# Kernel tuning notes

Hardware: AMD Instinct MI355X
Metric: run time of the kernel (lower is better)

Reference implementation:

```python
import jax, jax.numpy as jnp
import numpy as np
from jax import lax

B, L, D, H = 2, 4096, 1024, 16
K = 4            # short conv kernel size
HD = D // H      # head dim = 64
EPS = 1e-5


def causal_dw_conv(x, w):
    # depthwise causal conv: x [B,L,D], w [D,K]
    xp = jnp.pad(x, ((0, 0), (K - 1, 0), (0, 0)))
    out = xp[:, 0:L, :] * w[:, 0]
    for j in range(1, K):
        out = out + xp[:, j:j + L, :] * w[:, j]
    return out


def setup_inputs() -> dict:
    key = jax.random.key(0)
    ks = jax.random.split(key, 10)
    s = 0.02
    return {
        "hidden_states": jax.random.normal(ks[0], (B, L, D), jnp.float32),
        "Wq": jax.random.normal(ks[1], (D, D), jnp.float32) * s,
        "Wk": jax.random.normal(ks[2], (D, D), jnp.float32) * s,
        "Wv": jax.random.normal(ks[3], (D, D), jnp.float32) * s,
        "Wb": jax.random.normal(ks[4], (D, H), jnp.float32) * s,
        "conv_q": jax.random.normal(ks[5], (D, K), jnp.float32) * s,
        "conv_k": jax.random.normal(ks[6], (D, K), jnp.float32) * s,
        "conv_v": jax.random.normal(ks[7], (D, K), jnp.float32) * s,
        "o_norm_w": jnp.ones((HD,), jnp.float32),
        "Wo": jax.random.normal(ks[8], (D, D), jnp.float32) * s,
    }


def reference(hidden_states, Wq, Wk, Wv, Wb, conv_q, conv_k, conv_v, o_norm_w, Wo):
    x = hidden_states
    # projections + short causal conv with SiLU (qk_activation == 'silu')
    q = jax.nn.silu(causal_dw_conv(x @ Wq, conv_q))
    k = jax.nn.silu(causal_dw_conv(x @ Wk, conv_k))
    v = jax.nn.silu(causal_dw_conv(x @ Wv, conv_v))

    # [B,L,D] -> [L,B,H,hd] for the time scan
    def to_heads(t):
        return t.reshape(B, L, H, HD).transpose(1, 0, 2, 3)

    q, k, v = to_heads(q), to_heads(k), to_heads(v)

    # l2 qk-norm
    q = q / jnp.linalg.norm(q, axis=-1, keepdims=True)
    k = k / jnp.linalg.norm(k, axis=-1, keepdims=True)

    # beta gate [L,B,H]
    beta = jax.nn.sigmoid(x @ Wb).transpose(1, 0, 2)

    def step(S, inp):
        qt, kt, vt, bt = inp  # [B,H,hd] x3, [B,H]
        v_old = jnp.einsum('bhk,bhkv->bhv', kt, S)
        delta = (vt - v_old) * bt[..., None]
        S = S + jnp.einsum('bhk,bhv->bhkv', kt, delta)
        ot = jnp.einsum('bhk,bhkv->bhv', qt, S)
        return S, ot

    S0 = jnp.zeros((B, H, HD, HD), x.dtype)
    _, o = lax.scan(step, S0, (q, k, v, beta))  # o: [L,B,H,hd]
    o = o.transpose(1, 0, 2, 3)  # [B,L,H,hd]

    # per-head RMSNorm
    rms = jax.lax.rsqrt(jnp.mean(o * o, axis=-1, keepdims=True) + EPS)
    o = o * rms * o_norm_w

    return o.reshape(B, L, D) @ Wo
```

## Files before the change

### kernel.cpp

```cpp
#include <hip/hip_runtime.h>
#include <hip/hip_bf16.h>
#include <math.h>

#define BB 2
#define LL 4096
#define DD 1024
#define HH 16
#define HDIM 64
#define CC 64
#define NC 64
#define BH 32
#define GG 8
#define GS 8

typedef __attribute__((ext_vector_type(8))) short short8;
typedef __attribute__((ext_vector_type(4))) float f32x4;
typedef unsigned short u16;
typedef unsigned int u32;

__device__ __forceinline__ u16 f2bf(float f) {
    unsigned int u = __float_as_uint(f);
    unsigned int r = (u + 0x7fffu + ((u >> 16) & 1u)) >> 16;
    return (u16)r;
}
__device__ __forceinline__ float bf2f(u16 h) {
    return __uint_as_float((unsigned)h << 16);
}
__device__ __forceinline__ void split2(float x, u16& h, u16& l) {
    h = f2bf(x);
    l = f2bf(x - bf2f(h));
}
__device__ __forceinline__ u32 packhl(float x) {
    u16 h, l; split2(x, h, l);
    return (u32)h | ((u32)l << 16);
}
__device__ __forceinline__ float unpackhl(u32 v) {
    return bf2f((u16)v) + bf2f((u16)(v >> 16));
}
__device__ __forceinline__ float4 ld_bf4(const u16* p) {
    uint2 v = *(const uint2*)p;
    return make_float4(bf2f((u16)v.x), bf2f((u16)(v.x >> 16)),
                       bf2f((u16)v.y), bf2f((u16)(v.y >> 16)));
}

__device__ __forceinline__ void gld_lds16(const void* g, void* l) {
    __builtin_amdgcn_global_load_lds(
        (const __attribute__((address_space(1))) void*)g,
        (__attribute__((address_space(3))) void*)l, 16, 0, 0);
}

__device__ __forceinline__ int swz(int r, int c) {
    return (r << 6) + ((((c >> 2) ^ (r >> 2)) & 15) << 2) + (c & 3);
}
__device__ __forceinline__ int swze(int r, int c) {
    return (r << 6) + (c ^ (((r ^ (r >> 3)) & 7) << 3));
}

__device__ __forceinline__ void mm64(const u16* __restrict__ Ah, const u16* __restrict__ Al,
                                     const u16* __restrict__ Bh, const u16* __restrict__ Bl,
                                     f32x4* acc, int w, int lane) {
    const int ln = lane & 15, kg = (lane >> 4) * 8;
#pragma unroll
    for (int kb = 0; kb < 2; ++kb) {
        const int k0 = kb * 32 + kg;
        short8 ah = *(const short8*)&Ah[swze(w * 16 + ln, k0)];
        short8 al = *(const short8*)&Al[swze(w * 16 + ln, k0)];
#pragma unroll
        for (int j = 0; j < 4; ++j) {
            short8 bh = *(const short8*)&Bh[swze(j * 16 + ln, k0)];
            short8 bl = *(const short8*)&Bl[swze(j * 16 + ln, k0)];
            acc[j] = __builtin_amdgcn_mfma_f32_16x16x32_bf16(ah, bh, acc[j], 0, 0, 0);
            acc[j] = __builtin_amdgcn_mfma_f32_16x16x32_bf16(ah, bl, acc[j], 0, 0, 0);
            acc[j] = __builtin_amdgcn_mfma_f32_16x16x32_bf16(al, bh, acc[j], 0, 0, 0);
        }
    }
}
__device__ __forceinline__ void mm64_bb(const u16* __restrict__ Ah,
                                        const u16* __restrict__ Bh,
                                        f32x4* acc, int w, int lane) {
    const int ln = lane & 15, kg = (lane >> 4) * 8;
#pragma unroll
    for (int kb = 0; kb < 2; ++kb) {
        const int k0 = kb * 32 + kg;
        short8 ah = *(const short8*)&Ah[swze(w * 16 + ln, k0)];
#pragma unroll
        for (int j = 0; j < 4; ++j) {
            short8 bh = *(const short8*)&Bh[swze(j * 16 + ln, k0)];
            acc[j] = __builtin_amdgcn_mfma_f32_16x16x32_bf16(ah, bh, acc[j], 0, 0, 0);
        }
    }
}
__device__ __forceinline__ void mm64_ab(const u16* __restrict__ Ah,
                                        const u16* __restrict__ Bh, const u16* __restrict__ Bl,
                                        f32x4* acc, int w, int lane) {
    const int ln = lane & 15, kg = (lane >> 4) * 8;
#pragma unroll
    for (int kb = 0; kb < 2; ++kb) {
        const int k0 = kb * 32 + kg;
        short8 ah = *(const short8*)&Ah[swze(w * 16 + ln, k0)];
#pragma unroll
        for (int j = 0; j < 4; ++j) {
            short8 bh = *(const short8*)&Bh[swze(j * 16 + ln, k0)];
            short8 bl = *(const short8*)&Bl[swze(j * 16 + ln, k0)];
            acc[j] = __builtin_amdgcn_mfma_f32_16x16x32_bf16(ah, bh, acc[j], 0, 0, 0);
            acc[j] = __builtin_amdgcn_mfma_f32_16x16x32_bf16(ah, bl, acc[j], 0, 0, 0);
        }
    }
}
__device__ __forceinline__ void mm64_sb(const u16* __restrict__ Ah, const u16* __restrict__ Al,
                                        const u16* __restrict__ Bh,
                                        f32x4* acc, int w, int lane) {
    const int ln = lane & 15, kg = (lane >> 4) * 8;
#pragma unroll
    for (int kb = 0; kb < 2; ++kb) {
        const int k0 = kb * 32 + kg;
        short8 ah = *(const short8*)&Ah[swze(w * 16 + ln, k0)];
        short8 al = *(const short8*)&Al[swze(w * 16 + ln, k0)];
#pragma unroll
        for (int j = 0; j < 4; ++j) {
            short8 bh = *(const short8*)&Bh[swze(j * 16 + ln, k0)];
            acc[j] = __builtin_amdgcn_mfma_f32_16x16x32_bf16(ah, bh, acc[j], 0, 0, 0);
            acc[j] = __builtin_amdgcn_mfma_f32_16x16x32_bf16(al, bh, acc[j], 0, 0, 0);
        }
    }
}

__device__ __forceinline__ void g_to_ls_b(const u16* __restrict__ G16, u16* Ah, int tid) {
#pragma unroll
    for (int p = 0; p < 2; ++p) {
        int flat = p * 2048 + tid * 8;
        int r = flat >> 6, c = flat & 63;
        *(short8*)&Ah[swze(r, c)] = *(const short8*)&G16[flat];
    }
}

__device__ __forceinline__ void pload(uint4 pf[4], const u32* __restrict__ G, int tid) {
    pf[0] = *(const uint4*)&G[tid * 8];
    pf[1] = *(const uint4*)&G[tid * 8 + 4];
    pf[2] = *(const uint4*)&G[2048 + tid * 8];
    pf[3] = *(const uint4*)&G[2048 + tid * 8 + 4];
}
__device__ __forceinline__ void pstore_ls(const uint4 pf[4], u16* Ah, u16* Al, int tid) {
#pragma unroll
    for (int p = 0; p < 2; ++p) {
        int flat = p * 2048 + tid * 8;
        int r = flat >> 6, c = flat & 63;
        uint4 a = pf[2 * p], b = pf[2 * p + 1];
        short8 hi, lo;
        hi[0] = (short)(u16)a.x; hi[1] = (short)(u16)a.y;
        hi[2] = (short)(u16)a.z; hi[3] = (short)(u16)a.w;
        hi[4] = (short)(u16)b.x; hi[5] = (short)(u16)b.y;
        hi[6] = (short)(u16)b.z; hi[7] = (short)(u16)b.w;
        lo[0] = (short)(a.x >> 16); lo[1] = (short)(a.y >> 16);
        lo[2] = (short)(a.z >> 16); lo[3] = (short)(a.w >> 16);
        lo[4] = (short)(b.x >> 16); lo[5] = (short)(b.y >> 16);
        lo[6] = (short)(b.z >> 16); lo[7] = (short)(b.w >> 16);
        *(short8*)&Ah[swze(r, c)] = hi;
        *(short8*)&Al[swze(r, c)] = lo;
    }
}
__device__ __forceinline__ void gp_to_ls(const u32* __restrict__ G, u16* Ah, u16* Al, int tid) {
    uint4 pf[4];
    pload(pf, G, tid);
    pstore_ls(pf, Ah, Al, tid);
}

__device__ __forceinline__ void frag_to_ls(const f32x4* acc, u16* Ah, u16* Al, int w, int lane) {
    const int g = lane >> 4, ln = lane & 15;
#pragma unroll
    for (int j = 0; j < 4; ++j)
#pragma unroll
        for (int r = 0; r < 4; ++r) {
            int row = w * 16 + g * 4 + r, col = j * 16 + ln;
            u16 h, l; split2(acc[j][r], h, l);
            Ah[swze(row, col)] = h;
            Al[swze(row, col)] = l;
        }
}

__device__ __forceinline__ void gp_to_frag(const u32* __restrict__ G, f32x4* acc, int w, int lane) {
    const int g = lane >> 4, ln = lane & 15;
#pragma unroll
    for (int j = 0; j < 4; ++j)
#pragma unroll
        for (int r = 0; r < 4; ++r)
            acc[j][r] = unpackhl(G[(w * 16 + g * 4 + r) * 64 + j * 16 + ln]);
}
__device__ __forceinline__ void gp_add_frag(const u32* __restrict__ G, f32x4* acc, int w, int lane) {
    const int g = lane >> 4, ln = lane & 15;
#pragma unroll
    for (int j = 0; j < 4; ++j)
#pragma unroll
        for (int r = 0; r < 4; ++r)
            acc[j][r] += unpackhl(G[(w * 16 + g * 4 + r) * 64 + j * 16 + ln]);
}
__device__ __forceinline__ void frag_to_gp(const f32x4* acc, u32* __restrict__ G, int w, int lane) {
    const int g = lane >> 4, ln = lane & 15;
#pragma unroll
    for (int j = 0; j < 4; ++j)
#pragma unroll
        for (int r = 0; r < 4; ++r)
            G[(w * 16 + g * 4 + r) * 64 + j * 16 + ln] = packhl(acc[j][r]);
}

__global__ __launch_bounds__(256) void prep_k(const float* __restrict__ in,
                                              u16* __restrict__ out,
                                              const float* __restrict__ W0,
                                              const float* __restrict__ W1,
                                              const float* __restrict__ W2,
                                              const float* __restrict__ W3,
                                              u16* __restrict__ WT0) {
    __shared__ float t[32][33];
    const int bid = blockIdx.x;
    if (bid < 4096) {
        int i = (bid * 256 + threadIdx.x) * 8;
        float4 a = *(const float4*)&in[i];
        float4 b = *(const float4*)&in[i + 4];
        uint4 o;
        o.x = (unsigned)f2bf(a.x) | ((unsigned)f2bf(a.y) << 16);
        o.y = (unsigned)f2bf(a.z) | ((unsigned)f2bf(a.w) << 16);
        o.z = (unsigned)f2bf(b.x) | ((unsigned)f2bf(b.y) << 16);
        o.w = (unsigned)f2bf(b.z) | ((unsigned)f2bf(b.w) << 16);
        *(uint4*)&out[i] = o;
        return;
    }
    const int t2 = bid - 4096;
    const int which = t2 >> 10, rem = t2 & 1023;
    const int bx = (rem & 31) * 32, by = (rem >> 5) * 32;
    const float* W = (which == 0) ? W0 : (which == 1) ? W1 : (which == 2) ? W2 : W3;
    u16* WT = WT0 + (size_t)which * 1048576;
#pragma unroll
    for (int p = 0; p < 4; ++p) {
        int idx = p * 256 + threadIdx.x;
        int r = idx >> 5, cc = idx & 31;
        t[r][cc] = W[(size_t)(by + r) * 1024 + bx + cc];
    }
    __syncthreads();
#pragma unroll
    for (int p = 0; p < 4; ++p) {
        int idx = p * 256 + threadIdx.x;
        int r = idx >> 5, cc = idx & 31;
        WT[(size_t)(bx + r) * 1024 + by + cc] = f2bf(t[cc][r]);
    }
}

__device__ __forceinline__ void gemm_core256(const u16* A, const u16* BT,
                                             int m0, int n0, f32x4 acc[8][4]) {
    __shared__ __align__(16) short As[4][256 * 32];
    __shared__ __align__(16) short Bs[4][256 * 32];
    const int tid = threadIdx.x;
    const int lane = tid & 63, w = tid >> 6;
    const int wr = w >> 2, wc = w & 3;
    const int ln15 = lane & 15, kch = lane >> 4;
    const int erow = tid >> 2;
    const int ecol = (((tid & 3) ^ ((tid >> 3) & 3)) << 3);

#define STAGE256(buf, t)                                                      \
    {   const int k0_ = (t) * 32;                                             \
        _Pragma("unroll")                                                     \
        for (int rr = 0; rr < 2; ++rr) {                                      \
            gld_lds16(A  + (size_t)(m0 + rr * 128 + erow) * 1024 + k0_ + ecol,\
                      (short*)As[buf] + rr * 4096 + tid * 8);                 \
            gld_lds16(BT + (size_t)(n0 + rr * 128 + erow) * 1024 + k0_ + ecol,\
                      (short*)Bs[buf] + rr * 4096 + tid * 8);                 \
        } }

#define RF256(Fa, Fb, buf)                                                    \
    {   _Pragma("unroll")                                                     \
        for (int i = 0; i < 8; ++i) {                                         \
            int row = wr * 128 + i * 16 + ln15;                               \
            Fa[i] = *(const short8*)&As[buf][row * 32 + ((kch ^ ((row >> 1) & 3)) << 3)]; \
        }                                                                     \
        _Pragma("unroll")                                                     \
        for (int j = 0; j < 4; ++j) {                                         \
            int row = wc * 64 + j * 16 + ln15;                                \
            Fb[j] = *(const short8*)&Bs[buf][row * 32 + ((kch ^ ((row >> 1) & 3)) << 3)]; \
        } }

#define MM256(Fa, Fb)                                                         \
    {   __builtin_amdgcn_s_setprio(1);                                        \
        _Pragma("unroll")                                                     \
        for (int i = 0; i < 8; ++i)                                           \
            _Pragma("unroll")                                                 \
            for (int j = 0; j < 4; ++j)                                       \
                acc[i][j] = __builtin_amdgcn_mfma_f32_16x16x32_bf16(Fa[i], Fb[j], acc[i][j], 0, 0, 0); \
        __builtin_amdgcn_s_setprio(0); }

#define BODY256(t, Ca, Cb, Na, Nb)                                            \
    {   if ((t) + 3 < 32) STAGE256(((t) + 3) & 3, (t) + 3);                   \
        if ((t) < 29)       asm volatile("s_waitcnt vmcnt(8)" ::: "memory");  \
        else if ((t) == 29) asm volatile("s_waitcnt vmcnt(4)" ::: "memory");  \
        else if ((t) == 30) asm volatile("s_waitcnt vmcnt(0)" ::: "memory");  \
        asm volatile("s_waitcnt lgkmcnt(0)" ::: "memory");                    \
        __builtin_amdgcn_s_barrier();                                         \
        if ((t) < 31) RF256(Na, Nb, ((t) + 1) & 3);                           \
        MM256(Ca, Cb); }

    short8 Xa[8], Xb[4], Ya[8], Yb[4];
    STAGE256(0, 0);
    STAGE256(1, 1);
    STAGE256(2, 2);
    asm volatile("s_waitcnt vmcnt(8)" ::: "memory");
    __builtin_amdgcn_s_barrier();
    RF256(Xa, Xb, 0);
    for (int t2 = 0; t2 < 32; t2 += 2) {
        BODY256(t2, Xa, Xb, Ya, Yb);
        BODY256(t2 + 1, Ya, Yb, Xa, Xb);
    }
#undef STAGE256
#undef RF256
#undef MM256
#undef BODY256
}

__device__ __forceinline__ int xcd_swz(int lid, int nwg) {
    int q = nwg >> 3;
    return (lid & 7) * q + (lid >> 3);
}

__global__ __launch_bounds__(512, 2) void gemm_bf16(const u16* __restrict__ A,
                                                    const u16* __restrict__ BT,
                                                    float* __restrict__ C) {
    const int lid = blockIdx.y * 4 + blockIdx.x;
    const int sid = xcd_swz(lid, 128);
    const int m0 = (sid >> 2) * 256, n0 = (sid & 3) * 256;
    f32x4 acc[8][4] = {};
    gemm_core256(A, BT, m0, n0, acc);
    const int lane = threadIdx.x & 63, w = threadIdx.x >> 6;
    const int crow0 = m0 + (w >> 2) * 128 + (lane >> 4) * 4;
    const int ccol0 = n0 + (w & 3) * 64 + (lane & 15);
#pragma unroll
    for (int i = 0; i < 8; ++i)
#pragma unroll
        for (int j = 0; j < 4; ++j)
#pragma unroll
            for (int r = 0; r < 4; ++r)
                C[(size_t)(crow0 + i * 16 + r) * 1024 + ccol0 + j * 16] = acc[i][j][r];
}

__global__ __launch_bounds__(512, 2) void gemm_qkv(const u16* __restrict__ A,
                                                   const u16* __restrict__ WT0,
                                                   u16* __restrict__ xq16,
                                                   u16* __restrict__ xk16,
                                                   u16* __restrict__ xv16) {
    const int lid = blockIdx.y * 12 + blockIdx.x;
    const int sid = xcd_swz(lid, 384);
    const int lbx = sid % 12;
    const int which = lbx >> 2;
    const int n0 = (lbx & 3) * 256;
    const int m0 = (sid / 12) * 256;
    const u16* BT = WT0 + (size_t)which * 1048576;
    f32x4 acc[8][4] = {};
    gemm_core256(A, BT, m0, n0, acc);
    const int lane = threadIdx.x & 63, w = threadIdx.x >> 6;
    const int crow0 = m0 + (w >> 2) * 128 + (lane >> 4) * 4;
    const int ccol0 = n0 + (w & 3) * 64 + (lane & 15);
    u16* C16 = (which == 0) ? xq16 : (which == 1) ? xk16 : xv16;
#pragma unroll
    for (int i = 0; i < 8; ++i)
#pragma unroll
        for (int j = 0; j < 4; ++j)
#pragma unroll
            for (int r = 0; r < 4; ++r)
                C16[(size_t)(crow0 + i * 16 + r) * 1024 + ccol0 + j * 16] = f2bf(acc[i][j][r]);
}

__global__ __launch_bounds__(256) void beta_k(const float* __restrict__ X,
                                              const float* __restrict__ Wb,
                                              float* __restrict__ beta) {
    int idx = blockIdx.x * 256 + threadIdx.x;
    int row = idx >> 4, h = idx & 15;
    const float* xr = X + (size_t)row * DD;
    float s = 0.f;
    for (int k4 = 0; k4 < DD; k4 += 4) {
        float4 xv = *(const float4*)&xr[k4];
        s += xv.x * Wb[(k4 + 0) * HH + h];
        s += xv.y * Wb[(k4 + 1) * HH + h];
        s += xv.z * Wb[(k4 + 2) * HH + h];
        s += xv.w * Wb[(k4 + 3) * HH + h];
    }
    float bv = 1.f / (1.f + expf(-s));
    int b = row >> 12, l = row & (LL - 1);
    beta[((size_t)b * HH + h) * LL + l] = bv;
}

__global__ __launch_bounds__(256) void conv3_k(const u16* __restrict__ xq16,
                                               const u16* __restrict__ xk16,
                                               const u16* __restrict__ xv16,
                                               const float* __restrict__ cwq,
                                               const float* __restrict__ cwk,
                                               const float* __restrict__ cwv,
                                               u16* __restrict__ q16,
                                               u16* __restrict__ k16,
                                               u16* __restrict__ v16) {
    const int which = blockIdx.z;
    const float* cw = (which == 0) ? cwq : (which == 1) ? cwk : cwv;
    const int l0 = blockIdx.x * 16, b = blockIdx.y;
    const int tid = threadIdx.x;
    const int d0 = tid * 4;
    const float4 w0 = *(const float4*)&cw[(d0 + 0) * 4];
    const float4 w1 = *(const float4*)&cw[(d0 + 1) * 4];
    const float4 w2 = *(const float4*)&cw[(d0 + 2) * 4];
    const float4 w3 = *(const float4*)&cw[(d0 + 3) * 4];
    const int h = d0 >> 6, hd = d0 & 63;
    const u16* Xb = ((which == 0) ? xq16 : (which == 1) ? xk16 : xv16) + (size_t)b * LL * DD;
    u16* O16 = (which == 0) ? q16 : (which == 1) ? k16 : v16;
    float4 xm3 = make_float4(0, 0, 0, 0), xm2 = xm3, xm1 = xm3;
    if (l0 > 0) {
        xm3 = ld_bf4(&Xb[(size_t)(l0 - 3) * DD + d0]);
        xm2 = ld_bf4(&Xb[(size_t)(l0 - 2) * DD + d0]);
        xm1 = ld_bf4(&Xb[(size_t)(l0 - 1) * DD + d0]);
    }
#pragma unroll
    for (int t = 0; t < 16; ++t) {
        const int l = l0 + t;
        float4 xc = ld_bf4(&Xb[(size_t)l * DD + d0]);
        float a0 = xm3.x * w0.x + xm2.x * w0.y + xm1.x * w0.z + xc.x * w0.w;
        float a1 = xm3.y * w1.x + xm2.y * w1.y + xm1.y * w1.z + xc.y * w1.w;
        float a2 = xm3.z * w2.x + xm2.z * w2.y + xm1.z * w2.z + xc.z * w2.w;
        float a3 = xm3.w * w3.x + xm2.w * w3.y + xm1.w * w3.z + xc.w * w3.w;
        a0 = a0 / (1.f + expf(-a0));
        a1 = a1 / (1.f + expf(-a1));
        a2 = a2 / (1.f + expf(-a2));
        a3 = a3 / (1.f + expf(-a3));
        if (which < 2) {
            float s = a0 * a0 + a1 * a1 + a2 * a2 + a3 * a3;
            s += __shfl_xor(s, 1);
            s += __shfl_xor(s, 2);
            s += __shfl_xor(s, 4);
            s += __shfl_xor(s, 8);
            float sc = rsqrtf(s);
            a0 *= sc; a1 *= sc; a2 *= sc; a3 *= sc;
        }
        uint2 o;
        o.x = (unsigned)f2bf(a0) | ((unsigned)f2bf(a1) << 16);
        o.y = (unsigned)f2bf(a2) | ((unsigned)f2bf(a3) << 16);
        *(uint2*)&O16[(((size_t)b * HH + h) * LL + l) * 64 + hd] = o;
        xm3 = xm2; xm2 = xm1; xm1 = xc;
    }
}

__global__ __launch_bounds__(256) void phaseA6(const u16* __restrict__ kg16,
                                               const u16* __restrict__ vg16,
                                               const float* __restrict__ betag,
                                               u16* __restrict__ Wg16,
                                               u16* __restrict__ UgT16,
                                               u32* __restrict__ PallP,
                                               u32* __restrict__ BallTP) {
    __shared__ __align__(16) char pool[73728];
    u16* Kh   = (u16*)pool;
    u16* KTh  = (u16*)(pool + 8192);
    float* At = (float*)(pool + 16384);
    float* WU = (float*)(pool + 32768);
    u16* WTh  = (u16*)pool;
    u16* WTl  = (u16*)(pool + 16384);
    u16* UTh  = (u16*)(pool + 24576);
    u16* UTl  = (u16*)(pool + 65536);
    float* scr  = (float*)(pool + 32768);
    float* scrP = (float*)(pool + 49152);

    const int c = blockIdx.x, bh = blockIdx.y;
    const int tid = threadIdx.x, lane = tid & 63, w = tid >> 6;
    const int g = lane >> 4, ln = lane & 15;
    const int t0 = (tid >> 4) * 4, d4 = (tid & 15) * 4;
    const size_t base = ((size_t)bh * LL + (size_t)c * 64) * 64;
    const size_t obase = ((size_t)bh * NC + c) * 4096;
    const float* bet = betag + (size_t)bh * LL + (size_t)c * 64;

    g_to_ls_b(kg16 + base, Kh, tid);
    {
        u16 kv[4][4];
#pragma unroll
        for (int i = 0; i < 4; ++i) {
            uint2 v = *(const uint2*)&kg16[base + (size_t)(t0 + i) * 64 + d4];
            kv[i][0] = (u16)v.x; kv[i][1] = (u16)(v.x >> 16);
            kv[i][2] = (u16)v.y; kv[i][3] = (u16)(v.y >> 16);
        }
#pragma unroll
        for (int j = 0; j < 4; ++j) {
            uint2 hv;
            hv.x = (unsigned)kv[0][j] | ((unsigned)kv[1][j] << 16);
            hv.y = (unsigned)kv[2][j] | ((unsigned)kv[3][j] << 16);
            *(uint2*)&KTh[swze(d4 + j, t0)] = hv;
        }
    }
    __syncthreads();
    {
        f32x4 acc[4] = {};
        mm64_bb(Kh, Kh, acc, w, lane);
#pragma unroll
        for (int r = 0; r < 4; ++r) {
            int t = w * 16 + g * 4 + r;
            float bt = bet[t];
#pragma unroll
            for (int j = 0; j < 4; ++j) {
                int s = j * 16 + ln;
                At[t * 64 + s] = (s < t) ? bt * acc[j][r] : 0.f;
            }
        }
    }
#pragma unroll
    for (int p = 0; p < 8; ++p) {
        int flat = p * 1024 + tid * 4;
        int t = flat >> 7, j = flat & 127;
        float bt = bet[t];
        float4 src;
        if (j < 64) src = ld_bf4(&Kh[swze(t, j)]);
        else        src = ld_bf4(&vg16[base + (size_t)t * 64 + (j - 64)]);
        src.x *= bt; src.y *= bt; src.z *= bt; src.w *= bt;
        *(float4*)&WU[t * 128 + j] = src;
    }
    __syncthreads();
#pragma unroll
    for (int pb = 0; pb < 4; ++pb) {
        const int r0 = pb * 16;
        if (pb > 0) {
            const int col = tid & 127;
            const int rbase = r0 + (tid >> 7) * 8;
            float acc8[8] = {};
            for (int r = 0; r < r0; r += 4) {
                float u0 = WU[(r + 0) * 128 + col], u1 = WU[(r + 1) * 128 + col];
                float u2 = WU[(r + 2) * 128 + col], u3 = WU[(r + 3) * 128 + col];
#pragma unroll
                for (int i = 0; i < 8; ++i) {
                    float4 a4 = *(const float4*)&At[(rbase + i) * 64 + r];
                    acc8[i] += a4.x * u0 + a4.y * u1 + a4.z * u2 + a4.w * u3;
                }
            }
#pragma unroll
            for (int i = 0; i < 8; ++i) WU[(rbase + i) * 128 + col] -= acc8[i];
            __syncthreads();
        }
        if (tid < 128) {
            const int col = tid;
            float wv[16];
            wv[0] = WU[r0 * 128 + col];
#pragma unroll
            for (int t = 1; t < 16; ++t) {
                float a = WU[(r0 + t) * 128 + col];
#pragma unroll
                for (int r = 0; r < t; ++r) a -= At[(r0 + t) * 64 + r0 + r] * wv[r];
                wv[t] = a;
            }
#pragma unroll
            for (int t = 1; t < 16; ++t) WU[(r0 + t) * 128 + col] = wv[t];
        }
        __syncthreads();
    }
#pragma unroll
    for (int p = 0; p < 4; ++p) {
        int flat = p * 1024 + tid * 4;
        int t = flat >> 6, j = flat & 63;
        float4 v = *(const float4*)&WU[t * 128 + j];
        uint2 o;
        o.x = (unsigned)f2bf(v.x) | ((unsigned)f2bf(v.y) << 16);
        o.y = (unsigned)f2bf(v.z) | ((unsigned)f2bf(v.w) << 16);
        *(uint2*)&Wg16[obase + flat] = o;
    }
    {
        u16 h4[4][4], l4[4][4];
#pragma unroll
        for (int i = 0; i < 4; ++i) {
            float4 v = *(const float4*)&WU[(t0 + i) * 128 + d4];
            split2(v.x, h4[i][0], l4[i][0]); split2(v.y, h4[i][1], l4[i][1]);
            split2(v.z, h4[i][2], l4[i][2]); split2(v.w, h4[i][3], l4[i][3]);
        }
#pragma unroll
        for (int j = 0; j < 4; ++j) {
            uint2 hv, lv;
            hv.x = (unsigned)h4[0][j] | ((unsigned)h4[1][j] << 16);
            hv.y = (unsigned)h4[2][j] | ((unsigned)h4[3][j] << 16);
            lv.x = (unsigned)l4[0][j] | ((unsigned)l4[1][j] << 16);
            lv.y = (unsigned)l4[2][j] | ((unsigned)l4[3][j] << 16);
            *(uint2*)&WTh[swze(d4 + j, t0)] = hv;
            *(uint2*)&WTl[swze(d4 + j, t0)] = lv;
        }
#pragma unroll
        for (int i = 0; i < 4; ++i) {
            float4 v = *(const float4*)&WU[(t0 + i) * 128 + 64 + d4];
            split2(v.x, h4[i][0], l4[i][0]); split2(v.y, h4[i][1], l4[i][1]);
            split2(v.z, h4[i][2], l4[i][2]); split2(v.w, h4[i][3], l4[i][3]);
        }
#pragma unroll
        for (int j = 0; j < 4; ++j) {
            uint2 hv, lv;
            hv.x = (unsigned)h4[0][j] | ((unsigned)h4[1][j] << 16);
            hv.y = (unsigned)h4[2][j] | ((unsigned)h4[3][j] << 16);
            lv.x = (unsigned)l4[0][j] | ((unsigned)l4[1][j] << 16);
            lv.y = (unsigned)l4[2][j] | ((unsigned)l4[3][j] << 16);
            *(uint2*)&UTh[swze(d4 + j, t0)] = hv;
            *(uint2*)&UTl[swze(d4 + j, t0)] = lv;
        }
    }
    __syncthreads();
#pragma unroll
    for (int p = 0; p < 2; ++p) {
        int flat = p * 2048 + tid * 8;
        int n = flat >> 6, tt = flat & 63;
        *(short8*)&UgT16[obase + flat] = *(const short8*)&UTh[swze(n, tt)];
    }
    f32x4 aP[4] = {}, aB[4] = {};
    mm64_ab(KTh, WTh, WTl, aP, w, lane);
    mm64_ab(KTh, UTh, UTl, aB, w, lane);
#pragma unroll
    for (int j = 0; j < 4; ++j)
#pragma unroll
        for (int r = 0; r < 4; ++r) {
            int row = w * 16 + g * 4 + r, col = j * 16 + ln;
            scrP[swz(row, col)] = ((row == col) ? 1.f : 0.f) - aP[j][r];
            scr[swz(row, col)] = aB[j][r];
        }
    __syncthreads();
#pragma unroll
    for (int p = 0; p < 4; ++p) {
        int flat = p * 1024 + tid * 4;
        int rr = flat >> 6, cc = flat & 63;
        uint4 op;
        op.x = packhl(scrP[swz(rr, cc + 0)]);
        op.y = packhl(scrP[swz(rr, cc + 1)]);
        op.z = packhl(scrP[swz(rr, cc + 2)]);
        op.w = packhl(scrP[swz(rr, cc + 3)]);
        *(uint4*)&PallP[obase + flat] = op;
        uint4 ob4;
        ob4.x = packhl(scr[swz(cc + 0, rr)]);
        ob4.y = packhl(scr[swz(cc + 1, rr)]);
        ob4.z = packhl(scr[swz(cc + 2, rr)]);
        ob4.w = packhl(scr[swz(cc + 3, rr)]);
        *(uint4*)&BallTP[obase + flat] = ob4;
    }
}

__global__ __launch_bounds__(256) void compose4(const u32* __restrict__ PallP,
                                                const u32* __restrict__ BallTP,
                                                u32* __restrict__ PgP,
                                                u32* __restrict__ BgTP) {
    __shared__ __align__(16) char pool[81920];
    u16* Ph = (u16*)pool;
    u16* Pl = (u16*)(pool + 8192);
    u16* Bh = (u16*)(pool + 16384);
    u16* Bl = (u16*)(pool + 24576);
    u16* nh = (u16*)(pool + 32768);
    u16* nl = (u16*)(pool + 40960);
    float* scr = (float*)(pool + 49152);
    const int g = blockIdx.x, bh = blockIdx.y;
    const int tid = threadIdx.x, lane = tid & 63, w = tid >> 6;
    const int gi = lane >> 4, ln = lane & 15;
    const size_t base0 = ((size_t)bh * NC + (size_t)g * GS) * 4096;
    f32x4 mP[4], mB[4];
#pragma unroll
    for (int p = 0; p < 4; ++p) {
        int flat = p * 1024 + tid * 4;
        int r = flat >> 6, c4 = flat & 63;
        uint4 pk = *(const uint4*)&PallP[base0 + flat];
        *(float4*)&scr[swz(r, c4)] =
            make_float4(unpackhl(pk.x), unpackhl(pk.y), unpackhl(pk.z), unpackhl(pk.w));
    }
    gp_to_frag(BallTP + base0, mB, w, lane);
    __syncthreads();
#pragma unroll
    for (int j = 0; j < 4; ++j)
#pragma unroll
        for (int r = 0; r < 4; ++r) {
            int row = w * 16 + gi * 4 + r, col = j * 16 + ln;
            mP[j][r] = scr[swz(col, row)];
        }
    uint4 pf[4];
    pload(pf, PallP + base0 + 4096, tid);
    for (int s = 1; s < GS; ++s) {
        __syncthreads();
        frag_to_ls(mP, Ph, Pl, w, lane);
        frag_to_ls(mB, Bh, Bl, w, lane);
        pstore_ls(pf, nh, nl, tid);
        __syncthreads();
        if (s < GS - 1) pload(pf, PallP + base0 + (size_t)(s + 1) * 4096, tid);
        f32x4 aP[4] = {}, aB[4] = {};
        mm64(Ph, Pl, nh, nl, aP, w, lane);
        mm64(Bh, Bl, nh, nl, aB, w, lane);
        gp_add_frag(BallTP + base0 + (size_t)s * 4096, aB, w, lane);
#pragma unroll
        for (int j = 0; j < 4; ++j) { mP[j] = aP[j]; mB[j] = aB[j]; }
    }
    const size_t gbase = ((size_t)bh * GG + g) * 4096;
    frag_to_gp(mB, BgTP + gbase, w, lane);
    __syncthreads();
#pragma unroll
    for (int j = 0; j < 4; ++j)
#pragma unroll
        for (int r = 0; r < 4; ++r) {
            int row = w * 16 + gi * 4 + r, col = j * 16 + ln;
            scr[swz(row, col)] = mP[j][r];
        }
    __syncthreads();
#pragma unroll
    for (int p = 0; p < 4; ++p) {
        int flat = p * 1024 + tid * 4;
        int a = flat >> 6, b0 = flat & 63;
        uint4 o;
        o.x = packhl(scr[swz(b0 + 0, a)]);
        o.y = packhl(scr[swz(b0 + 1, a)]);
        o.z = packhl(scr[swz(b0 + 2, a)]);
        o.w = packhl(scr[swz(b0 + 3, a)]);
        *(uint4*)&PgP[gbase + flat] = o;
    }
}

__global__ __launch_bounds__(256) void scanG4(const u32* __restrict__ PgP,
                                              const u32* __restrict__ BgTP,
                                              u32* __restrict__ SallTP) {
    __shared__ __align__(16) char pool[32768];
    u16* Sh = (u16*)pool;
    u16* Sl = (u16*)(pool + 8192);
    u16* nh = (u16*)(pool + 16384);
    u16* nl = (u16*)(pool + 24576);
    const int bh = blockIdx.x;
    const int tid = threadIdx.x, lane = tid & 63, w = tid >> 6;
    f32x4 mS[4] = {};
    for (int g = 0; g < GG; ++g) {
        const size_t sbase = ((size_t)bh * NC + (size_t)g * GS) * 4096;
        frag_to_gp(mS, SallTP + sbase, w, lane);
        if (g == GG - 1) break;
        __syncthreads();
        frag_to_ls(mS, Sh, Sl, w, lane);
        gp_to_ls(PgP + ((size_t)bh * GG + g) * 4096, nh, nl, tid);
        __syncthreads();
        f32x4 a[4] = {};
        mm64(Sh, Sl, nh, nl, a, w, lane);
        gp_add_frag(BgTP + ((size_t)bh * GG + g) * 4096, a, w, lane);
#pragma unroll
        for (int j = 0; j < 4; ++j) mS[j] = a[j];
    }
}

__global__ __launch_bounds__(256) void rollout4(const u32* __restrict__ PallP,
                                                const u32* __restrict__ BallTP,
                                                u32* __restrict__ SallTP) {
    __shared__ __align__(16) char pool[32768];
    u16* Sh = (u16*)pool;
    u16* Sl = (u16*)(pool + 8192);
    u16* nh = (u16*)(pool + 16384);
    u16* nl = (u16*)(pool + 24576);
    const int g = blockIdx.x, bh = blockIdx.y;
    const int tid = threadIdx.x, lane = tid & 63, w = tid >> 6;
    const size_t base0 = ((size_t)bh * NC + (size_t)g * GS) * 4096;
    f32x4 mS[4];
    gp_to_frag(SallTP + base0, mS, w, lane);
    uint4 pf[4];
    pload(pf, PallP + base0, tid);
    for (int j = 1; j < GS; ++j) {
        __syncthreads();
        frag_to_ls(mS, Sh, Sl, w, lane);
        pstore_ls(pf, nh, nl, tid);
        __syncthreads();
        if (j < GS - 1) pload(pf, PallP + base0 + (size_t)j * 4096, tid);
        f32x4 a[4] = {};
        mm64(Sh, Sl, nh, nl, a, w, lane);
        gp_add_frag(BallTP + base0 + (size_t)(j - 1) * 4096, a, w, lane);
#pragma unroll
        for (int jj = 0; jj < 4; ++jj) mS[jj] = a[jj];
        frag_to_gp(mS, SallTP + base0 + (size_t)j * 4096, w, lane);
    }
}

__global__ __launch_bounds__(256) void phaseO6(const u16* __restrict__ Wg16,
                                               const u16* __restrict__ UgT16,
                                               const u16* __restrict__ qg16,
                                               const u16* __restrict__ kg16,
                                               const u32* __restrict__ SallTP,
                                               const float* __restrict__ nw,
                                               u16* __restrict__ ob) {
    __shared__ __align__(16) char pool[57344];
    u16* Qh = (u16*)pool;
    u16* Kh = (u16*)(pool + 8192);
    u16* Wh = (u16*)(pool + 16384);
    u16* Wl = (u16*)(pool + 24576);
    u16* Sh = (u16*)(pool + 32768);
    u16* Sl = (u16*)(pool + 40960);
    u16* Dl = (u16*)(pool + 49152);
    u16* Dh = Kh;
    u16* Mh = Wh; u16* Ml = Wl;
    const int c = blockIdx.x, bh = blockIdx.y;
    const int b = bh >> 4, h = bh & 15;
    const int tid = threadIdx.x, lane = tid & 63, w = tid >> 6;
    const int gi = lane >> 4, ln = lane & 15;
    const size_t tbase = ((size_t)bh * NC + c) * 4096;
    const size_t qkbase = ((size_t)bh * LL + (size_t)c * 64) * 64;
    g_to_ls_b(qg16 + qkbase, Qh, tid);
    g_to_ls_b(kg16 + qkbase, Kh, tid);
    g_to_ls_b(Wg16 + tbase, Wh, tid);
    gp_to_ls(SallTP + tbase, Sh, Sl, tid);
    __syncthreads();
    f32x4 aM[4] = {}, aD[4] = {};
    mm64_bb(Qh, Kh, aM, w, lane);
    mm64_sb(Sh, Sl, Wh, aD, w, lane);
    __syncthreads();
#pragma unroll
    for (int j = 0; j < 4; ++j)
#pragma unroll
        for (int r = 0; r < 4; ++r) {
            int row = w * 16 + gi * 4 + r, col = j * 16 + ln;
            float mv = (col <= row) ? aM[j][r] : 0.f;
            u16 mh_, ml_; split2(mv, mh_, ml_);
            Mh[swze(row, col)] = mh_;
            Ml[swze(row, col)] = ml_;
            float dv = bf2f(UgT16[tbase + (size_t)row * 64 + col]) - aD[j][r];
            u16 dh_, dl_; split2(dv, dh_, dl_);
            Dh[swze(row, col)] = dh_;
            Dl[swze(row, col)] = dl_;
        }
    __syncthreads();
    f32x4 aO[4] = {};
    mm64_ab(Qh, Sh, Sl, aO, w, lane);
    mm64(Mh, Ml, Dh, Dl, aO, w, lane);
    float nwv[4];
#pragma unroll
    for (int j = 0; j < 4; ++j) nwv[j] = nw[j * 16 + ln];
#pragma unroll
    for (int r = 0; r < 4; ++r) {
        float ss = 0.f;
#pragma unroll
        for (int j = 0; j < 4; ++j) ss += aO[j][r] * aO[j][r];
        ss += __shfl_xor(ss, 1);
        ss += __shfl_xor(ss, 2);
        ss += __shfl_xor(ss, 4);
        ss += __shfl_xor(ss, 8);
        float rms = rsqrtf(ss * (1.f / 64.f) + 1e-5f);
        int row = w * 16 + gi * 4 + r;
        size_t orow = ((size_t)b * LL + (size_t)c * 64 + row) * DD + (size_t)h * 64;
#pragma unroll
        for (int j = 0; j < 4; ++j)
            ob[orow + j * 16 + ln] = f2bf(aO[j][r] * rms * nwv[j]);
    }
}

extern "C" void kernel_launch(void* const* d_in, const int* in_sizes, int n_in,
                              void* d_out, int out_size, void* d_ws, size_t ws_size,
                              hipStream_t stream) {
    const float* x  = (const float*)d_in[0];
    const float* Wq = (const float*)d_in[1];
    const float* Wk = (const float*)d_in[2];
    const float* Wv = (const float*)d_in[3];
    const float* Wb = (const float*)d_in[4];
    const float* cq = (const float*)d_in[5];
    const float* ck = (const float*)d_in[6];
    const float* cv = (const float*)d_in[7];
    const float* nw = (const float*)d_in[8];
    const float* Wo = (const float*)d_in[9];
    float* out = (float*)d_out;
    float* ws = (float*)d_ws;

    const size_t SZ = (size_t)BB * LL * DD;
    u16* xv16    = (u16*)ws;
    u16* v16     = (u16*)(ws + SZ);
    u16* Wg16    = (u16*)(ws + 2 * SZ);
    u16* UgT16   = (u16*)(ws + 2 * SZ) + SZ;
    u32* SallTP  = (u32*)(ws + 4 * SZ);
    u16* xb   = (u16*)(ws + 5 * SZ);
    u16* q16  = xb;
    u16* xq16 = (u16*)(ws + 5 * SZ) + SZ;
    u16* xk16 = (u16*)(ws + 5 * SZ) + 2 * SZ;
    u16* k16  = (u16*)(ws + 5 * SZ) + 3 * SZ;
    float* beta = ws + 7 * SZ;
    u16* wqT  = (u16*)(beta + (size_t)BH * LL);
    u32* PgP  = (u32*)(wqT + (size_t)4 * 1048576);
    u32* BgTP = PgP + 1048576;

    u32* PallP  = (u32*)ws;
    u32* BallTP = (u32*)out;
    u16* ob   = (u16*)(ws + SZ);
    u16* woT  = wqT + (size_t)3 * 1048576;

    dim3 blk(256);

    prep_k<<<dim3(8192), blk, 0, stream>>>(x, xb, Wq, Wk, Wv, Wo, wqT);
    gemm_qkv<<<dim3(12, 32), dim3(512), 0, stream>>>(xb, wqT, xq16, xk16, xv16);
    beta_k<<<dim3(512), blk, 0, stream>>>(x, Wb, beta);
    conv3_k<<<dim3(LL / 16, BB, 3), blk, 0, stream>>>(xq16, xk16, xv16, cq, ck, cv, q16, k16, v16);
    phaseA6<<<dim3(NC, BH), blk, 0, stream>>>(k16, v16, beta, Wg16, UgT16, PallP, BallTP);
    compose4<<<dim3(GG, BH), blk, 0, stream>>>(PallP, BallTP, PgP, BgTP);
    scanG4<<<dim3(BH), blk, 0, stream>>>(PgP, BgTP, SallTP);
    rollout4<<<dim3(GG, BH), blk, 0, stream>>>(PallP, BallTP, SallTP);
    phaseO6<<<dim3(NC, BH), blk, 0, stream>>>(Wg16, UgT16, q16, k16, SallTP, nw, ob);
    gemm_bf16<<<dim3(4, 32), dim3(512), 0, stream>>>(ob, woT, out);
}
```

Measured before the change: 336.7 us.

## Use bf16 input for beta, single-bf16 U in phaseA, stage U via LDS in phaseO

The beta gate projection now reads the bf16 copy of the input instead of fp32, which halves the bytes it loads. In phaseA6 the U matrix is stored as a single bf16 array rather than a hi/lo split pair, so one of the two split-precision matmuls becomes a plain bf16 matmul and shared memory shrinks to 64KB. phaseO6 now loads the U tile into LDS with a coalesced bulk copy instead of issuing a scattered global read per element. The cost is some accuracy in beta and in the B matrix, and phaseO6's shared memory grows to 64KB, which may lower its occupancy.

```diff
diff --git a/kernel.cpp b/kernel.cpp
--- a/kernel.cpp
+++ b/kernel.cpp
@@ -365,19 +365,18 @@
                 C16[(size_t)(crow0 + i * 16 + r) * 1024 + ccol0 + j * 16] = f2bf(acc[i][j][r]);
 }
 
-__global__ __launch_bounds__(256) void beta_k(const float* __restrict__ X,
+__global__ __launch_bounds__(256) void beta_k(const u16* __restrict__ X16,
                                               const float* __restrict__ Wb,
                                               float* __restrict__ beta) {
     int idx = blockIdx.x * 256 + threadIdx.x;
     int row = idx >> 4, h = idx & 15;
-    const float* xr = X + (size_t)row * DD;
+    const u16* xr = X16 + (size_t)row * DD;
     float s = 0.f;
-    for (int k4 = 0; k4 < DD; k4 += 4) {
-        float4 xv = *(const float4*)&xr[k4];
-        s += xv.x * Wb[(k4 + 0) * HH + h];
-        s += xv.y * Wb[(k4 + 1) * HH + h];
-        s += xv.z * Wb[(k4 + 2) * HH + h];
-        s += xv.w * Wb[(k4 + 3) * HH + h];
+    for (int k8 = 0; k8 < DD; k8 += 8) {
+        short8 xv = *(const short8*)&xr[k8];
+#pragma unroll
+        for (int e = 0; e < 8; ++e)
+            s += bf2f((u16)xv[e]) * Wb[(k8 + e) * HH + h];
     }
     float bv = 1.f / (1.f + expf(-s));
     int b = row >> 12, l = row & (LL - 1);
@@ -447,7 +446,7 @@
                                                u16* __restrict__ UgT16,
                                                u32* __restrict__ PallP,
                                                u32* __restrict__ BallTP) {
-    __shared__ __align__(16) char pool[73728];
+    __shared__ __align__(16) char pool[65536];
     u16* Kh   = (u16*)pool;
     u16* KTh  = (u16*)(pool + 8192);
     float* At = (float*)(pool + 16384);
@@ -455,7 +454,6 @@
     u16* WTh  = (u16*)pool;
     u16* WTl  = (u16*)(pool + 16384);
     u16* UTh  = (u16*)(pool + 24576);
-    u16* UTl  = (u16*)(pool + 65536);
     float* scr  = (float*)(pool + 32768);
     float* scrP = (float*)(pool + 49152);
 
@@ -578,18 +576,15 @@
 #pragma unroll
         for (int i = 0; i < 4; ++i) {
             float4 v = *(const float4*)&WU[(t0 + i) * 128 + 64 + d4];
-            split2(v.x, h4[i][0], l4[i][0]); split2(v.y, h4[i][1], l4[i][1]);
-            split2(v.z, h4[i][2], l4[i][2]); split2(v.w, h4[i][3], l4[i][3]);
+            h4[i][0] = f2bf(v.x); h4[i][1] = f2bf(v.y);
+            h4[i][2] = f2bf(v.z); h4[i][3] = f2bf(v.w);
         }
 #pragma unroll
         for (int j = 0; j < 4; ++j) {
-            uint2 hv, lv;
+            uint2 hv;
             hv.x = (unsigned)h4[0][j] | ((unsigned)h4[1][j] << 16);
             hv.y = (unsigned)h4[2][j] | ((unsigned)h4[3][j] << 16);
-            lv.x = (unsigned)l4[0][j] | ((unsigned)l4[1][j] << 16);
-            lv.y = (unsigned)l4[2][j] | ((unsigned)l4[3][j] << 16);
             *(uint2*)&UTh[swze(d4 + j, t0)] = hv;
-            *(uint2*)&UTl[swze(d4 + j, t0)] = lv;
         }
     }
     __syncthreads();
@@ -601,7 +596,7 @@
     }
     f32x4 aP[4] = {}, aB[4] = {};
     mm64_ab(KTh, WTh, WTl, aP, w, lane);
-    mm64_ab(KTh, UTh, UTl, aB, w, lane);
+    mm64_bb(KTh, UTh, aB, w, lane);
 #pragma unroll
     for (int j = 0; j < 4; ++j)
 #pragma unroll
@@ -768,7 +763,7 @@
                                                const u32* __restrict__ SallTP,
                                                const float* __restrict__ nw,
                                                u16* __restrict__ ob) {
-    __shared__ __align__(16) char pool[57344];
+    __shared__ __align__(16) char pool[65536];
     u16* Qh = (u16*)pool;
     u16* Kh = (u16*)(pool + 8192);
     u16* Wh = (u16*)(pool + 16384);
@@ -776,6 +771,7 @@
     u16* Sh = (u16*)(pool + 32768);
     u16* Sl = (u16*)(pool + 40960);
     u16* Dl = (u16*)(pool + 49152);
+    u16* Uh = (u16*)(pool + 57344);
     u16* Dh = Kh;
     u16* Mh = Wh; u16* Ml = Wl;
     const int c = blockIdx.x, bh = blockIdx.y;
@@ -787,6 +783,7 @@
     g_to_ls_b(qg16 + qkbase, Qh, tid);
     g_to_ls_b(kg16 + qkbase, Kh, tid);
     g_to_ls_b(Wg16 + tbase, Wh, tid);
+    g_to_ls_b(UgT16 + tbase, Uh, tid);
     gp_to_ls(SallTP + tbase, Sh, Sl, tid);
     __syncthreads();
     f32x4 aM[4] = {}, aD[4] = {};
@@ -802,7 +799,7 @@
             u16 mh_, ml_; split2(mv, mh_, ml_);
             Mh[swze(row, col)] = mh_;
             Ml[swze(row, col)] = ml_;
-            float dv = bf2f(UgT16[tbase + (size_t)row * 64 + col]) - aD[j][r];
+            float dv = bf2f(Uh[swze(row, col)]) - aD[j][r];
             u16 dh_, dl_; split2(dv, dh_, dl_);
             Dh[swze(row, col)] = dh_;
             Dl[swze(row, col)] = dl_;
@@ -873,7 +870,7 @@
 
     prep_k<<<dim3(8192), blk, 0, stream>>>(x, xb, Wq, Wk, Wv, Wo, wqT);
     gemm_qkv<<<dim3(12, 32), dim3(512), 0, stream>>>(xb, wqT, xq16, xk16, xv16);
-    beta_k<<<dim3(512), blk, 0, stream>>>(x, Wb, beta);
+    beta_k<<<dim3(512), blk, 0, stream>>>(xb, Wb, beta);
     conv3_k<<<dim3(LL / 16, BB, 3), blk, 0, stream>>>(xq16, xk16, xv16, cq, ck, cv, q16, k16, v16);
     phaseA6<<<dim3(NC, BH), blk, 0, stream>>>(k16, v16, beta, Wg16, UgT16, PallP, BallTP);
     compose4<<<dim3(GG, BH), blk, 0, stream>>>(PallP, BallTP, PgP, BgTP);
```

Result: faster. 318.9 us (-5.3%).
